# Optimization experiments

Measured on AMD Instinct MI355X. Metric: run time of the kernel, lower is better.

Reference implementation:

```python
import jax, jax.numpy as jnp
import numpy as np

T, B = 512, 64
DIM_INPUT, DIM_LATENT, VOCAB = 512, 1024, 50257


def setup_inputs() -> dict:
    key = jax.random.key(0)
    ks = jax.random.split(key, 12)
    s = 0.02
    return {
        "X": jax.random.randint(ks[0], (T, B), 0, VOCAB, dtype=jnp.int32),
        "h": jax.random.normal(ks[1], (B, DIM_LATENT), dtype=jnp.float32),
        "emb": jax.random.normal(ks[2], (VOCAB, DIM_INPUT), dtype=jnp.float32) * s,
        "Wf": jax.random.normal(ks[3], (DIM_LATENT + DIM_INPUT, DIM_LATENT), dtype=jnp.float32) * s,
        "bf": jnp.zeros((DIM_LATENT,), dtype=jnp.float32),
        "Wi": jax.random.normal(ks[4], (DIM_LATENT + DIM_INPUT, DIM_LATENT), dtype=jnp.float32) * s,
        "bi": jnp.zeros((DIM_LATENT,), dtype=jnp.float32),
        "Wc": jax.random.normal(ks[5], (DIM_LATENT + DIM_INPUT, DIM_LATENT), dtype=jnp.float32) * s,
        "bc": jnp.zeros((DIM_LATENT,), dtype=jnp.float32),
        "Wo": jax.random.normal(ks[6], (DIM_LATENT + DIM_INPUT, DIM_LATENT), dtype=jnp.float32) * s,
        "bo": jnp.zeros((DIM_LATENT,), dtype=jnp.float32),
    }


def reference(X, h, emb, Wf, bf, Wi, bi, Wc, bc, Wo, bo):
    # X: [T, B] int tokens; h: [B, dim_latent]
    xe = emb[X]  # [T, B, dim_input] embedding gather
    c0 = jnp.zeros_like(h)

    def step(carry, x_t):
        h_prev, c_prev = carry
        m = jnp.concatenate([h_prev, x_t], axis=1)  # [B, dl+di]
        ft = jax.nn.sigmoid(m @ Wf + bf)
        it = jax.nn.sigmoid(m @ Wi + bi)
        ct = ft * c_prev + it * jnp.tanh(m @ Wc + bc)
        ot = jax.nn.sigmoid(m @ Wo + bo)
        ht = ot * jnp.tanh(ct)
        return (ht, ct), ht

    (_, _), H = jax.lax.scan(step, (h, c0), xe)
    return H  # [T, B, dim_latent]
```

## Files before the change

kernel.cpp:

```cpp
#include <hip/hip_runtime.h>


namespace {
constexpr int T_STEPS = 512;
constexpr int BATCH   = 64;
constexpr int DI      = 512;
constexpr int DL      = 1024;
constexpr int NKC     = 48;
constexpr int NKC_H   = 32;
constexpr int NBLK    = 256;
constexpr int NTHR    = 256;
constexpr int FPAD    = 32;
}

typedef __attribute__((ext_vector_type(8))) short bf16x8;
typedef __attribute__((ext_vector_type(8))) unsigned short u16x8;
typedef __attribute__((ext_vector_type(4))) float f32x4;
typedef __attribute__((ext_vector_type(4))) unsigned int u32x4;
typedef __attribute__((ext_vector_type(2))) unsigned int u32x2;

__device__ __forceinline__ unsigned short f2bf(float x){
  unsigned int u = __float_as_uint(x);
  return (unsigned short)((u + 0x7FFFu + ((u >> 16) & 1u)) >> 16);
}
__device__ __forceinline__ float bf2f(unsigned short b){
  return __uint_as_float(((unsigned int)b) << 16);
}
__device__ __forceinline__ float fast_sigmoid(float v){
  return __fdividef(1.f, 1.f + __expf(-v));
}
__device__ __forceinline__ float fast_tanh(float v){
  v = fminf(fmaxf(v, -15.f), 15.f);
  float t = __expf(2.f * v);
  return __fdividef(t - 1.f, t + 1.f);
}

__global__ void prep_xe(const int* __restrict__ X, const float* __restrict__ emb,
                        unsigned short* __restrict__ xe){
  int i = blockIdx.x * blockDim.x + threadIdx.x;
  const int total = T_STEPS * BATCH * DI / 8;
  if (i >= total) return;
  int row = i >> 6;
  int seg = i & 63;
  int tok = X[row];
  const float* src = emb + (long long)tok * DI + seg * 8;
  float4 v0 = *(const float4*)src;
  float4 v1 = *(const float4*)(src + 4);
  u16x8 o;
  o[0]=f2bf(v0.x); o[1]=f2bf(v0.y); o[2]=f2bf(v0.z); o[3]=f2bf(v0.w);
  o[4]=f2bf(v1.x); o[5]=f2bf(v1.y); o[6]=f2bf(v1.z); o[7]=f2bf(v1.w);
  *(u16x8*)(xe + (long long)row * DI + seg * 8) = o;
}

__global__ void prep_w(const float* __restrict__ Wf, const float* __restrict__ Wi,
                       const float* __restrict__ Wc, const float* __restrict__ Wo,
                       unsigned short* __restrict__ W_hi, unsigned short* __restrict__ W_lo){
  int idx = blockIdx.x * blockDim.x + threadIdx.x;
  if (idx >= 256 * NKC * 64) return;
  int lane = idx & 63;
  int kc   = (idx >> 6) % NKC;
  int bk   = idx / (64 * NKC);
  int lc = lane & 15, kg = lane >> 4;
  int g  = lc >> 2;
  int jl = bk * 4 + (lc & 3);
  const float* Wg = (g == 0) ? Wf : ((g == 1) ? Wi : ((g == 2) ? Wc : Wo));
  int kbase = kc * 32 + kg * 8;
  u16x8 hi, lo;
#pragma unroll
  for (int j = 0; j < 8; j++){
    float wv = Wg[(long long)(kbase + j) * DL + jl];
    unsigned short h = f2bf(wv);
    hi[j] = h;
    lo[j] = f2bf(wv - bf2f(h));
  }
  *(u16x8*)(W_hi + ((long long)(bk * NKC + kc) * 64 + lane) * 8) = hi;
  if (kc < NKC_H)
    *(u16x8*)(W_lo + ((long long)(bk * NKC_H + kc) * 64 + lane) * 8) = lo;
}

__global__ void prep_h(const float* __restrict__ h0,
                       const float* __restrict__ bf_, const float* __restrict__ bi_,
                       const float* __restrict__ bc_, const float* __restrict__ bo_,
                       unsigned short* __restrict__ hRing,
                       float* __restrict__ bias_pack, unsigned int* __restrict__ bar){
  int i = blockIdx.x * blockDim.x + threadIdx.x;
  if (i < BATCH * DL) hRing[i] = f2bf(h0[i]);
  if (i < 4096){
    int r = i & 3, g = (i >> 2) & 3, bk = i >> 4;
    const float* bg = (g == 0) ? bf_ : ((g == 1) ? bi_ : ((g == 2) ? bc_ : bo_));
    bias_pack[i] = bg[bk * 4 + r];
  }
  if (i < 8 * FPAD) bar[i] = 0u;
}

template<bool CACHED>
__launch_bounds__(NTHR, 1)
__global__ void lstm_persist(const unsigned short* __restrict__ xe,
                             const unsigned short* __restrict__ W_hi,
                             const unsigned short* __restrict__ W_lo,
                             unsigned short* __restrict__ hRing,
                             const float* __restrict__ bias_pack,
                             float* __restrict__ out,
                             unsigned int* __restrict__ bar){
  extern __shared__ unsigned short lds[];
  unsigned short* lds_hi = lds;
  unsigned short* lds_lo = lds + NKC * 512;
  __shared__ unsigned short stage_h[BATCH * 4];
  __shared__ float          stage_o[BATCH * 4];
  const int tid  = threadIdx.x;
  const int bk   = blockIdx.x;
  const int w    = tid >> 6;
  const int lane = tid & 63;

  const uint4* srcHi = (const uint4*)(W_hi + (size_t)bk * NKC * 512);
  uint4* dHi = (uint4*)lds_hi;
  for (int i = tid; i < 3072; i += NTHR) dHi[i] = srcHi[i];
  const uint4* srcLo = (const uint4*)(W_lo + (size_t)bk * NKC_H * 512);
  uint4* dLo = (uint4*)lds_lo;
  for (int i = tid; i < 2048; i += NTHR) dLo[i] = srcLo[i];
  __syncthreads();

  const int lc = lane & 15;
  const int kg = lane >> 4;
  const int g  = lc >> 2;
  const int rowb = (w << 4) + lc;
  const float bias = bias_pack[bk * 16 + lc];
  const int srcBase = (lane & 48) | (lc & 3);
  const int hOff = rowb * DL + kg * 8;
  const int xOff = rowb * DI + kg * 8;
  unsigned int* myCtr = bar + (bk & 7) * FPAD;
  unsigned int* pollp = bar + (lane & 7) * FPAD;
  float cr0 = 0.f, cr1 = 0.f, cr2 = 0.f, cr3 = 0.f;

  f32x4 acc0 = {0.f,0.f,0.f,0.f}, acc1 = {0.f,0.f,0.f,0.f};
  f32x4 acc2 = {0.f,0.f,0.f,0.f}, acc3 = {0.f,0.f,0.f,0.f};

#define XSTEP(KC, ACC) {                                                        \
    bf16x8 ax = *(const bf16x8*)(xRow + (KC) * 32);                             \
    bf16x8 bh = *(const bf16x8*)(lds_hi + (NKC_H + (KC)) * 512 + lane * 8);     \
    ACC = __builtin_amdgcn_mfma_f32_16x16x32_bf16(ax, bh, ACC, 0, 0, 0); }
#define HSTEP2(KC, ACC) {                                                       \
    bf16x8 ah = *(const bf16x8*)&hv[KC];                                        \
    bf16x8 bh = *(const bf16x8*)(lds_hi + (KC) * 512 + lane * 8);               \
    bf16x8 bl = *(const bf16x8*)(lds_lo + (KC) * 512 + lane * 8);               \
    ACC = __builtin_amdgcn_mfma_f32_16x16x32_bf16(ah, bh, ACC, 0, 0, 0);        \
    ACC = __builtin_amdgcn_mfma_f32_16x16x32_bf16(ah, bl, ACC, 0, 0, 0); }
#define LOADHC(I, OFFSTR)                                                       \
    asm volatile("global_load_dwordx4 %0, %1, off offset:" OFFSTR               \
                 : "=v"(hv[I]) : "v"(hbase));
#define LOADHU(I, OFFSTR)                                                       \
    asm volatile("global_load_dwordx4 %0, %1, off offset:" OFFSTR " sc0 sc1"    \
                 : "=v"(hv[I]) : "v"(hbase));

  {
    const unsigned short* xRow = xe + xOff;
#pragma unroll
    for (int kc = 0; kc < 16; kc += 4){
      XSTEP(kc, acc0) XSTEP(kc + 1, acc1) XSTEP(kc + 2, acc2) XSTEP(kc + 3, acc3)
    }
  }

#pragma unroll 1
  for (int t = 0; t < T_STEPS; ++t){
    if (t > 0 && w == 0){
      const unsigned tgt = 32u * (unsigned)t;
      int spin = 0;
      for (;;){
        unsigned v = __hip_atomic_load(pollp, __ATOMIC_RELAXED, __HIP_MEMORY_SCOPE_AGENT);
        if (__all((v >= tgt) ? 1 : 0)) break;
        __builtin_amdgcn_s_sleep(2);
        if (++spin > (1 << 16)) break;
      }
    }
    __syncthreads();

    const int slotR = CACHED ? t       : (t & 1);
    const int slotW = CACHED ? (t + 1) : ((t + 1) & 1);
    unsigned short* hWr = hRing + (size_t)slotW * (BATCH * DL);
    float* out_t = out + (size_t)t * (BATCH * DL);

    u32x4 hv[32];
    const unsigned short* hbase = hRing + (size_t)slotR * (BATCH * DL) + hOff;
    if constexpr (CACHED){
      LOADHC( 0,"0")    LOADHC( 1,"64")   LOADHC( 2,"128")  LOADHC( 3,"192")
      LOADHC( 4,"256")  LOADHC( 5,"320")  LOADHC( 6,"384")  LOADHC( 7,"448")
      LOADHC( 8,"512")  LOADHC( 9,"576")  LOADHC(10,"640")  LOADHC(11,"704")
      LOADHC(12,"768")  LOADHC(13,"832")  LOADHC(14,"896")  LOADHC(15,"960")
      LOADHC(16,"1024") LOADHC(17,"1088") LOADHC(18,"1152") LOADHC(19,"1216")
      LOADHC(20,"1280") LOADHC(21,"1344") LOADHC(22,"1408") LOADHC(23,"1472")
      LOADHC(24,"1536") LOADHC(25,"1600") LOADHC(26,"1664") LOADHC(27,"1728")
      LOADHC(28,"1792") LOADHC(29,"1856") LOADHC(30,"1920") LOADHC(31,"1984")
    } else {
      LOADHU( 0,"0")    LOADHU( 1,"64")   LOADHU( 2,"128")  LOADHU( 3,"192")
      LOADHU( 4,"256")  LOADHU( 5,"320")  LOADHU( 6,"384")  LOADHU( 7,"448")
      LOADHU( 8,"512")  LOADHU( 9,"576")  LOADHU(10,"640")  LOADHU(11,"704")
      LOADHU(12,"768")  LOADHU(13,"832")  LOADHU(14,"896")  LOADHU(15,"960")
      LOADHU(16,"1024") LOADHU(17,"1088") LOADHU(18,"1152") LOADHU(19,"1216")
      LOADHU(20,"1280") LOADHU(21,"1344") LOADHU(22,"1408") LOADHU(23,"1472")
      LOADHU(24,"1536") LOADHU(25,"1600") LOADHU(26,"1664") LOADHU(27,"1728")
      LOADHU(28,"1792") LOADHU(29,"1856") LOADHU(30,"1920") LOADHU(31,"1984")
    }
    asm volatile("s_waitcnt vmcnt(0)" ::: "memory");
    __builtin_amdgcn_sched_barrier(0);

#pragma unroll
    for (int kc = 0; kc < NKC_H; kc += 4){
      HSTEP2(kc, acc0) HSTEP2(kc + 1, acc1) HSTEP2(kc + 2, acc2) HSTEP2(kc + 3, acc3)
    }
    f32x4 acc = (acc0 + acc1) + (acc2 + acc3);

    float creg[4] = {cr0, cr1, cr2, cr3};
#pragma unroll
    for (int r = 0; r < 4; r++){
      float v = acc[r] + bias;
      float vF = __shfl(v, srcBase);
      float vI = __shfl(v, srcBase + 4);
      float vC = __shfl(v, srcBase + 8);
      float vO = __shfl(v, srcBase + 12);
      if (g == 0){
        int b = (w << 4) | (kg << 2) | r;
        float ft = fast_sigmoid(vF);
        float it = fast_sigmoid(vI);
        float gt = fast_tanh(vC);
        float ot = fast_sigmoid(vO);
        float cn = ft * creg[r] + it * gt;
        creg[r] = cn;
        float hn = ot * fast_tanh(cn);
        int si = (b << 2) | (lc & 3);
        stage_h[si] = f2bf(hn);
        stage_o[si] = hn;
      }
    }
    cr0 = creg[0]; cr1 = creg[1]; cr2 = creg[2]; cr3 = creg[3];

    __syncthreads();

    if (w == 0){
      u32x2  hv2 = *(const u32x2*)&stage_h[lane << 2];
      f32x4  ov  = *(const f32x4*)&stage_o[lane << 2];
      *(float4*)(out_t + lane * DL + (bk << 2)) = *(const float4*)&ov;
      unsigned short* hdst = hWr + lane * DL + (bk << 2);
      asm volatile("global_store_dwordx2 %0, %1, off sc0 sc1"
                   :: "v"(hdst), "v"(hv2) : "memory");
      asm volatile("s_waitcnt vmcnt(0)" ::: "memory");
      __builtin_amdgcn_sched_barrier(0);
      if (tid == 0)
        __hip_atomic_fetch_add(myCtr, 1u, __ATOMIC_RELAXED, __HIP_MEMORY_SCOPE_AGENT);
    }

    acc0 = (f32x4){0.f,0.f,0.f,0.f}; acc1 = (f32x4){0.f,0.f,0.f,0.f};
    acc2 = (f32x4){0.f,0.f,0.f,0.f}; acc3 = (f32x4){0.f,0.f,0.f,0.f};
    if (t + 1 < T_STEPS){
      const unsigned short* xRow = xe + (size_t)(t + 1) * BATCH * DI + xOff;
#pragma unroll
      for (int kc = 0; kc < 16; kc += 4){
        XSTEP(kc, acc0) XSTEP(kc + 1, acc1) XSTEP(kc + 2, acc2) XSTEP(kc + 3, acc3)
      }
    }
  }
#undef XSTEP
#undef HSTEP2
#undef LOADHC
#undef LOADHU
}

extern "C" void kernel_launch(void* const* d_in, const int* in_sizes, int n_in,
                              void* d_out, int out_size, void* d_ws, size_t ws_size,
                              hipStream_t stream){
  const int*   X   = (const int*)d_in[0];
  const float* h0  = (const float*)d_in[1];
  const float* emb = (const float*)d_in[2];
  const float* Wf  = (const float*)d_in[3];
  const float* bf_ = (const float*)d_in[4];
  const float* Wi  = (const float*)d_in[5];
  const float* bi_ = (const float*)d_in[6];
  const float* Wc  = (const float*)d_in[7];
  const float* bc_ = (const float*)d_in[8];
  const float* Wo  = (const float*)d_in[9];
  const float* bo_ = (const float*)d_in[10];
  float* out = (float*)d_out;

  const size_t SLOT = (size_t)BATCH * DL;
  const size_t base_need =
      sizeof(unsigned short) * ((size_t)T_STEPS * BATCH * DI
                              + (size_t)256 * NKC * 512
                              + (size_t)256 * NKC_H * 512)
    + sizeof(float) * 4096
    + sizeof(unsigned int) * 8 * FPAD + 4096;
  const size_t ring_full = sizeof(unsigned short) * SLOT * (size_t)(T_STEPS + 1);
  const bool cached = ws_size >= base_need + ring_full;
  const size_t ring_elems = cached ? SLOT * (size_t)(T_STEPS + 1) : SLOT * 2;

  char* ws = (char*)d_ws;
  size_t off = 0;
  auto alloc = [&](size_t bytes) -> void* {
    void* p = ws + off;
    off = (off + bytes + 255) & ~((size_t)255);
    return p;
  };
  unsigned short* xe        = (unsigned short*)alloc(sizeof(unsigned short) * (size_t)T_STEPS * BATCH * DI);
  unsigned short* W_hi      = (unsigned short*)alloc(sizeof(unsigned short) * (size_t)256 * NKC * 512);
  unsigned short* W_lo      = (unsigned short*)alloc(sizeof(unsigned short) * (size_t)256 * NKC_H * 512);
  unsigned short* hRing     = (unsigned short*)alloc(sizeof(unsigned short) * ring_elems);
  float*          bias_pack = (float*)alloc(sizeof(float) * 4096);
  unsigned int*   bar       = (unsigned int*)alloc(sizeof(unsigned int) * 8 * FPAD);
  (void)in_sizes; (void)n_in; (void)out_size;

  static bool attr_set = false;
  if (!attr_set){
    hipFuncSetAttribute((const void*)lstm_persist<true>,
                        hipFuncAttributeMaxDynamicSharedMemorySize, 160 * 1024);
    hipFuncSetAttribute((const void*)lstm_persist<false>,
                        hipFuncAttributeMaxDynamicSharedMemorySize, 160 * 1024);
    attr_set = true;
  }

  hipLaunchKernelGGL(prep_xe, dim3(8192), dim3(256), 0, stream, X, emb, xe);
  hipLaunchKernelGGL(prep_w,  dim3(3072), dim3(256), 0, stream, Wf, Wi, Wc, Wo, W_hi, W_lo);
  hipLaunchKernelGGL(prep_h,  dim3(256),  dim3(256), 0, stream, h0, bf_, bi_, bc_, bo_,
                     hRing, bias_pack, bar);
  if (cached)
    hipLaunchKernelGGL((lstm_persist<true>),  dim3(NBLK), dim3(NTHR), 80 * 1024, stream,
                       xe, W_hi, W_lo, hRing, bias_pack, out, bar);
  else
    hipLaunchKernelGGL((lstm_persist<false>), dim3(NBLK), dim3(NTHR), 80 * 1024, stream,
                       xe, W_hi, W_lo, hRing, bias_pack, out, bar);
}
```

Before: 4.268 ms.

## Split per-step grid barrier into two half-barriers overlapping h loads

Changes the counter mapping so each 32-block group increments one of 8 counters (bk>>5), letting blocks wait only for the producers of the first half of h before issuing those loads, then wait on the second half's counters before loading the rest. This is meant to overlap h-ring reads with the tail of the global barrier instead of waiting for all blocks. It also shortens the sleep interval and raises the spin limit. It adds a second __syncthreads and polling round per step, and the counter-to-column mapping must line up with which blocks write which h columns; if it does not, loads could read stale data.

```diff
diff --git a/kernel.cpp b/kernel.cpp
--- a/kernel.cpp
+++ b/kernel.cpp
@@ -128,8 +128,9 @@
   const int srcBase = (lane & 48) | (lc & 3);
   const int hOff = rowb * DL + kg * 8;
   const int xOff = rowb * DI + kg * 8;
-  unsigned int* myCtr = bar + (bk & 7) * FPAD;
-  unsigned int* pollp = bar + (lane & 7) * FPAD;
+  unsigned int* myCtr  = bar + (bk >> 5) * FPAD;
+  unsigned int* pollA  = bar + (lane & 3) * FPAD;
+  unsigned int* pollB  = bar + (4 + (lane & 3)) * FPAD;
   float cr0 = 0.f, cr1 = 0.f, cr2 = 0.f, cr3 = 0.f;
 
   f32x4 acc0 = {0.f,0.f,0.f,0.f}, acc1 = {0.f,0.f,0.f,0.f};
@@ -151,6 +152,16 @@
 #define LOADHU(I, OFFSTR)                                                       \
     asm volatile("global_load_dwordx4 %0, %1, off offset:" OFFSTR " sc0 sc1"    \
                  : "=v"(hv[I]) : "v"(hbase));
+#define LOAD_A(M)                                                               \
+    M( 0,"0")    M( 1,"64")   M( 2,"128")  M( 3,"192")                          \
+    M( 4,"256")  M( 5,"320")  M( 6,"384")  M( 7,"448")                          \
+    M( 8,"512")  M( 9,"576")  M(10,"640")  M(11,"704")                          \
+    M(12,"768")  M(13,"832")  M(14,"896")  M(15,"960")
+#define LOAD_B(M)                                                               \
+    M(16,"1024") M(17,"1088") M(18,"1152") M(19,"1216")                         \
+    M(20,"1280") M(21,"1344") M(22,"1408") M(23,"1472")                         \
+    M(24,"1536") M(25,"1600") M(26,"1664") M(27,"1728")                         \
+    M(28,"1792") M(29,"1856") M(30,"1920") M(31,"1984")
 
   {
     const unsigned short* xRow = xe + xOff;
@@ -166,10 +177,10 @@
       const unsigned tgt = 32u * (unsigned)t;
       int spin = 0;
       for (;;){
-        unsigned v = __hip_atomic_load(pollp, __ATOMIC_RELAXED, __HIP_MEMORY_SCOPE_AGENT);
+        unsigned v = __hip_atomic_load(pollA, __ATOMIC_RELAXED, __HIP_MEMORY_SCOPE_AGENT);
         if (__all((v >= tgt) ? 1 : 0)) break;
-        __builtin_amdgcn_s_sleep(2);
-        if (++spin > (1 << 16)) break;
+        __builtin_amdgcn_s_sleep(1);
+        if (++spin > (1 << 17)) break;
       }
     }
     __syncthreads();
@@ -181,25 +192,21 @@
 
     u32x4 hv[32];
     const unsigned short* hbase = hRing + (size_t)slotR * (BATCH * DL) + hOff;
-    if constexpr (CACHED){
-      LOADHC( 0,"0")    LOADHC( 1,"64")   LOADHC( 2,"128")  LOADHC( 3,"192")
-      LOADHC( 4,"256")  LOADHC( 5,"320")  LOADHC( 6,"384")  LOADHC( 7,"448")
-      LOADHC( 8,"512")  LOADHC( 9,"576")  LOADHC(10,"640")  LOADHC(11,"704")
-      LOADHC(12,"768")  LOADHC(13,"832")  LOADHC(14,"896")  LOADHC(15,"960")
-      LOADHC(16,"1024") LOADHC(17,"1088") LOADHC(18,"1152") LOADHC(19,"1216")
-      LOADHC(20,"1280") LOADHC(21,"1344") LOADHC(22,"1408") LOADHC(23,"1472")
-      LOADHC(24,"1536") LOADHC(25,"1600") LOADHC(26,"1664") LOADHC(27,"1728")
-      LOADHC(28,"1792") LOADHC(29,"1856") LOADHC(30,"1920") LOADHC(31,"1984")
-    } else {
-      LOADHU( 0,"0")    LOADHU( 1,"64")   LOADHU( 2,"128")  LOADHU( 3,"192")
-      LOADHU( 4,"256")  LOADHU( 5,"320")  LOADHU( 6,"384")  LOADHU( 7,"448")
-      LOADHU( 8,"512")  LOADHU( 9,"576")  LOADHU(10,"640")  LOADHU(11,"704")
-      LOADHU(12,"768")  LOADHU(13,"832")  LOADHU(14,"896")  LOADHU(15,"960")
-      LOADHU(16,"1024") LOADHU(17,"1088") LOADHU(18,"1152") LOADHU(19,"1216")
-      LOADHU(20,"1280") LOADHU(21,"1344") LOADHU(22,"1408") LOADHU(23,"1472")
-      LOADHU(24,"1536") LOADHU(25,"1600") LOADHU(26,"1664") LOADHU(27,"1728")
-      LOADHU(28,"1792") LOADHU(29,"1856") LOADHU(30,"1920") LOADHU(31,"1984")
-    }
+    if constexpr (CACHED){ LOAD_A(LOADHC) } else { LOAD_A(LOADHU) }
+
+    if (t > 0 && w == 0){
+      const unsigned tgt = 32u * (unsigned)t;
+      int spin = 0;
+      for (;;){
+        unsigned v = __hip_atomic_load(pollB, __ATOMIC_RELAXED, __HIP_MEMORY_SCOPE_AGENT);
+        if (__all((v >= tgt) ? 1 : 0)) break;
+        __builtin_amdgcn_s_sleep(1);
+        if (++spin > (1 << 17)) break;
+      }
+    }
+    __syncthreads();
+
+    if constexpr (CACHED){ LOAD_B(LOADHC) } else { LOAD_B(LOADHU) }
     asm volatile("s_waitcnt vmcnt(0)" ::: "memory");
     __builtin_amdgcn_sched_barrier(0);
 
@@ -262,6 +269,8 @@
 #undef HSTEP2
 #undef LOADHC
 #undef LOADHU
+#undef LOAD_A
+#undef LOAD_B
 }
 
 extern "C" void kernel_launch(void* const* d_in, const int* in_sizes, int n_in,
```

Result: slower. 4.413 ms (+3.4%).
